# Optimization experiments

Hardware: AMD Instinct MI355X
Metric: run time of the kernel (lower is better)

## Reference

```python
import jax, jax.numpy as jnp
import numpy as np
import math

B, S, D, H = 2, 2048, 1024, 16
DK = D // H


def setup_inputs() -> dict:
    key = jax.random.key(0)
    ks = jax.random.split(key, 8)
    s = 1.0 / math.sqrt(D)
    inp = {
        "query": jax.random.normal(ks[0], (B, S, D), jnp.float32),
        "key": jax.random.normal(ks[1], (B, S, D), jnp.float32),
        "value": jax.random.normal(ks[2], (B, S, D), jnp.float32),
        # causal mask: (1, 1, S, S), 1 where attention allowed
        "mask": jnp.tril(jnp.ones((S, S), jnp.int32))[None, None, :, :],
        "Wq": jax.random.normal(ks[3], (D, D), jnp.float32) * s,
        "Wk": jax.random.normal(ks[4], (D, D), jnp.float32) * s,
        "Wv": jax.random.normal(ks[5], (D, D), jnp.float32) * s,
        "Wo": jax.random.normal(ks[6], (D, D), jnp.float32) * s,
    }
    return inp


def reference(query, key, value, mask, Wq, Wk, Wv, Wo):
    # nn.Linear(bias=False): y = x @ W.T
    def proj_heads(x, W):
        y = jnp.einsum("bsd,ed->bse", x, W)          # (B,S,D)
        return y.reshape(B, -1, H, DK).transpose(0, 2, 1, 3)  # (B,H,S,DK)

    q = proj_heads(query, Wq)
    k = proj_heads(key, Wk)
    v = proj_heads(value, Wv)

    scale = jnp.asarray(math.sqrt(DK), q.dtype)
    scores = jnp.einsum("bhqd,bhkd->bhqk", q, k) / scale  # (B,H,S,S)
    scores = jnp.where(mask == 0, -jnp.inf, scores)
    attn = jax.nn.softmax(scores, axis=-1)
    # dropout p=0.0 (eval): identity
    out = jnp.einsum("bhqk,bhkd->bhqd", attn, v)          # (B,H,S,DK)
    concat = out.transpose(0, 2, 1, 3).reshape(B, -1, D)  # (B,S,D)
    return jnp.einsum("bsd,ed->bse", concat, Wo)
```

## Files before the change

kernel.cpp:

```cpp
#include <hip/hip_runtime.h>
#include <hip/hip_bf16.h>

#define B_ 2
#define S_ 2048
#define D_ 1024
#define H_ 16
#define DK_ 64

typedef __hip_bfloat16 bf16;
typedef __attribute__((ext_vector_type(8))) short bf16x8;
typedef __attribute__((ext_vector_type(4))) short bf16x4;
typedef __attribute__((ext_vector_type(4))) float f32x4;

#define GLDS16(g, l)                                                     \
    __builtin_amdgcn_global_load_lds(                                    \
        (const __attribute__((address_space(1))) void*)(g),              \
        (__attribute__((address_space(3))) void*)(l), 16, 0, 0)

#define MFMA_K32(a, b, c) __builtin_amdgcn_mfma_f32_16x16x32_bf16(a, b, c, 0, 0, 0)
#define MFMA_K16(a, b, c) __builtin_amdgcn_mfma_f32_16x16x16bf16_1k(a, b, c, 0, 0, 0)
#define EXP2F(x) __builtin_amdgcn_exp2f(x)

__global__ __launch_bounds__(256) void cvt_all(
    const float* __restrict__ q, const float* __restrict__ k, const float* __restrict__ v,
    const float* __restrict__ w0, const float* __restrict__ w1,
    const float* __restrict__ w2, const float* __restrict__ w3,
    bf16* __restrict__ oq, bf16* __restrict__ ok, bf16* __restrict__ ov,
    bf16* __restrict__ o0, bf16* __restrict__ o1, bf16* __restrict__ o2,
    bf16* __restrict__ o3) {
    int bid = blockIdx.x;
    const float* src; bf16* dst; int base;
    if      (bid < 2048) { src = q;  dst = oq; base = bid; }
    else if (bid < 4096) { src = k;  dst = ok; base = bid - 2048; }
    else if (bid < 6144) { src = v;  dst = ov; base = bid - 4096; }
    else if (bid < 6656) { src = w0; dst = o0; base = bid - 6144; }
    else if (bid < 7168) { src = w1; dst = o1; base = bid - 6656; }
    else if (bid < 7680) { src = w2; dst = o2; base = bid - 7168; }
    else                 { src = w3; dst = o3; base = bid - 7680; }
    int i = (base * 256 + threadIdx.x) * 8;
    float4 a = *(const float4*)(src + i);
    float4 b = *(const float4*)(src + i + 4);
    __align__(16) bf16 o[8];
    o[0] = __float2bfloat16(a.x); o[1] = __float2bfloat16(a.y);
    o[2] = __float2bfloat16(a.z); o[3] = __float2bfloat16(a.w);
    o[4] = __float2bfloat16(b.x); o[5] = __float2bfloat16(b.y);
    o[6] = __float2bfloat16(b.z); o[7] = __float2bfloat16(b.w);
    *(bf16x8*)(dst + i) = *(const bf16x8*)o;
}

__device__ __forceinline__ void proj_loop32(const bf16* __restrict__ X,
                                            const bf16* __restrict__ W,
                                            int m0, int n0, bf16* As, bf16* Bs,
                                            f32x4 (&acc)[4][4]) {
    const int K = D_;
    const int tid = threadIdx.x;
    const int lane = tid & 63, wave = tid >> 6;
    const int lm = lane & 15, quad = lane >> 4;
    const int wr = wave >> 1, wc = wave & 1;

    auto stage = [&](int t, int bf) {
        int k0 = t * 32;
        bf16* Ab = As + bf * (128 * 32);
        bf16* Bb = Bs + bf * (128 * 32);
#pragma unroll
        for (int i = 0; i < 2; ++i) {
            int s = i * 256 + tid;
            int row = s >> 2, c = (s & 3) ^ (row & 3);
            GLDS16(X + (size_t)(m0 + row) * K + k0 + c * 8, Ab + s * 8);
        }
#pragma unroll
        for (int i = 0; i < 2; ++i) {
            int s = i * 256 + tid;
            int row = s >> 2, c = (s & 3) ^ (row & 3);
            GLDS16(W + (size_t)(n0 + row) * K + k0 + c * 8, Bb + s * 8);
        }
    };

    stage(0, 0);
    for (int t = 0; t < K / 32; ++t) {
        __syncthreads();
        if (t + 1 < K / 32) stage(t + 1, (t + 1) & 1);
        const bf16* Ab = As + (t & 1) * (128 * 32);
        const bf16* Bb = Bs + (t & 1) * (128 * 32);
        bf16x8 aF[4], bF[4];
#pragma unroll
        for (int mt = 0; mt < 4; ++mt) {
            int row = wr * 64 + mt * 16 + lm;
            aF[mt] = *(const bf16x8*)(Ab + row * 32 + ((quad ^ (row & 3)) * 8));
        }
#pragma unroll
        for (int nt = 0; nt < 4; ++nt) {
            int row = wc * 64 + nt * 16 + lm;
            bF[nt] = *(const bf16x8*)(Bb + row * 32 + ((quad ^ (row & 3)) * 8));
        }
#pragma unroll
        for (int mt = 0; mt < 4; ++mt)
#pragma unroll
            for (int nt = 0; nt < 4; ++nt)
                acc[mt][nt] = MFMA_K32(aF[mt], bF[nt], acc[mt][nt]);
    }
}

__global__ __launch_bounds__(256) void proj_qkv(
    const bf16* __restrict__ qx, const bf16* __restrict__ kx, const bf16* __restrict__ vx,
    const bf16* __restrict__ wq, const bf16* __restrict__ wk, const bf16* __restrict__ wv,
    bf16* __restrict__ qb, bf16* __restrict__ kb, bf16* __restrict__ vtb) {
    __shared__ __align__(16) bf16 As[2 * 128 * 32];
    __shared__ __align__(16) bf16 Bs[2 * 128 * 32];
    const int L = (int)blockIdx.x;
    const int tile = (L & 7) * 96 + (L >> 3);
    const int z = tile >> 8;
    const int rem = tile & 255;
    const int n0 = (rem & 7) * 128;
    const int m0 = (rem >> 3) * 128;
    const bf16* X = (z == 0) ? qx : (z == 1) ? kx : vx;
    const bf16* W = (z == 0) ? wq : (z == 1) ? wk : wv;
    f32x4 acc[4][4] = {};
    proj_loop32(X, W, m0, n0, As, Bs, acc);

    const int lane = threadIdx.x & 63, wave = threadIdx.x >> 6;
    const int lm = lane & 15, quad = lane >> 4;
    const int wr = wave >> 1, wc = wave & 1;
#pragma unroll
    for (int mt = 0; mt < 4; ++mt) {
        int mbase = m0 + wr * 64 + mt * 16 + quad * 4;
#pragma unroll
        for (int nt = 0; nt < 4; ++nt) {
            int n = n0 + wc * 64 + nt * 16 + lm;
            if (z == 2) {
                int b = mbase >> 11, s = mbase & (S_ - 1);
                unsigned short u[4];
#pragma unroll
                for (int r = 0; r < 4; ++r) {
                    bf16 hv = __float2bfloat16(acc[mt][nt][r]);
                    u[r] = *(unsigned short*)&hv;
                }
                ushort4 pk = {u[0], u[1], u[2], u[3]};
                *(ushort4*)(vtb + ((size_t)(b * 1024 + n) * S_ + s)) = pk;
            } else {
                bf16* Y = z ? kb : qb;
#pragma unroll
                for (int r = 0; r < 4; ++r)
                    Y[(size_t)(mbase + r) * D_ + n] = __float2bfloat16(acc[mt][nt][r]);
            }
        }
    }
}

__global__ __launch_bounds__(256) void proj_o(const bf16* __restrict__ X,
                                              const bf16* __restrict__ W,
                                              float* __restrict__ Y) {
    __shared__ __align__(16) bf16 As[2 * 128 * 32];
    __shared__ __align__(16) bf16 Bs[2 * 128 * 32];
    const int L = (int)blockIdx.x;
    const int tile = (L & 7) * 32 + (L >> 3);
    const int n0 = (tile & 7) * 128;
    const int m0 = (tile >> 3) * 128;
    f32x4 acc[4][4] = {};
    proj_loop32(X, W, m0, n0, As, Bs, acc);

    const int lane = threadIdx.x & 63, wave = threadIdx.x >> 6;
    const int lm = lane & 15, quad = lane >> 4;
    const int wr = wave >> 1, wc = wave & 1;
#pragma unroll
    for (int mt = 0; mt < 4; ++mt) {
        int mbase = m0 + wr * 64 + mt * 16 + quad * 4;
#pragma unroll
        for (int nt = 0; nt < 4; ++nt) {
            int n = n0 + wc * 64 + nt * 16 + lm;
#pragma unroll
            for (int r = 0; r < 4; ++r)
                Y[(size_t)(mbase + r) * D_ + n] = acc[mt][nt][r];
        }
    }
}

__global__ __launch_bounds__(512) void attn_kernel(const bf16* __restrict__ Q,
                                                   const bf16* __restrict__ Kb,
                                                   const bf16* __restrict__ VT,
                                                   bf16* __restrict__ O) {
    __shared__ __align__(16) bf16 kt[2][128 * 64];
    __shared__ __align__(16) bf16 vt[2][64 * 128];

    const int tid = threadIdx.x;
    const int lane = tid & 63, wave = tid >> 6;
    const int lm = lane & 15, quad = lane >> 4;
    const int f = (int)blockIdx.x;
    const int cls = f & 7;
    const int t = f >> 3;
    const int qi = 15 - (t >> 2);
    const int combo = cls + 8 * (t & 3);
    const int b = combo >> 4, h = combo & 15;
    const int q0 = qi * 128 + wave * 16;

    const size_t bhoff = (size_t)b * S_ * D_ + (size_t)h * DK_;
    const bf16* vtb = VT + ((size_t)b * 1024 + h * DK_) * S_;

    const bf16* qp = Q + bhoff + (size_t)(q0 + lm) * D_ + quad * 8;
    bf16x8 aq0 = *(const bf16x8*)(qp);
    bf16x8 aq1 = *(const bf16x8*)(qp + 32);

    f32x4 oacc[4] = {};
    float lsum = 0.f;
    const float cexp = 0.125f * 1.44269504f;

    auto stage = [&](int i, int bf) {
        int j0s = i * 128;
#pragma unroll
        for (int ii = 0; ii < 2; ++ii) {
            int s = ii * 512 + tid;
            int j = s >> 3, c = (s & 7) ^ (j & 7);
            GLDS16(Kb + bhoff + (size_t)(j0s + j) * D_ + c * 8, kt[bf] + s * 8);
        }
#pragma unroll
        for (int ii = 0; ii < 2; ++ii) {
            int s = ii * 512 + tid;
            int d = s >> 4, c = (s & 15) ^ (d & 15);
            GLDS16(vtb + (size_t)d * S_ + j0s + c * 8, vt[bf] + s * 8);
        }
    };

    auto chunk = [&](const bf16* ktb, const bf16* vtl, int st, bool mk) {
        int j = st * 16 + lm;
        bf16x8 bk0 = *(const bf16x8*)(ktb + (((j << 3) | (quad ^ (j & 7))) * 8));
        bf16x8 bk1 = *(const bf16x8*)(ktb + (((j << 3) | ((4 + quad) ^ (j & 7))) * 8));
        f32x4 z = {};
        z = MFMA_K32(bk0, aq0, z);
        z = MFMA_K32(bk1, aq1, z);
        bf16x4 pa;
        float rs = 0.f;
#pragma unroll
        for (int r = 0; r < 4; ++r) {
            float p = EXP2F(z[r] * cexp);
            if (mk && (quad * 4 + r > lm)) p = 0.f;
            rs += p;
            bf16 hv = __float2bfloat16(p);
            pa[r] = *(short*)&hv;
        }
        lsum += rs;
#pragma unroll
        for (int dt = 0; dt < 4; ++dt) {
            int d = dt * 16 + lm;
            int cl = st * 2 + (quad >> 1);
            bf16x4 bv = *(const bf16x4*)(vtl + d * 128 +
                                         ((cl ^ (d & 15)) * 8 + (quad & 1) * 4));
            oacc[dt] = MFMA_K16(pa, bv, oacc[dt]);
        }
    };

    stage(0, 0);

    for (int i = 0; i <= qi; ++i) {
        __syncthreads();
        if (i < qi) stage(i + 1, (i + 1) & 1);
        const bf16* ktb = kt[i & 1];
        const bf16* vtl = vt[i & 1];
        if (i < qi) {
#pragma unroll
            for (int st = 0; st < 8; ++st) chunk(ktb, vtl, st, false);
        } else {
            for (int st = 0; st < wave; ++st) chunk(ktb, vtl, st, false);
            chunk(ktb, vtl, wave, true);
        }
    }

    float l = lsum;
    l += __shfl_xor(l, 16, 64);
    l += __shfl_xor(l, 32, 64);
#pragma unroll
    for (int r = 0; r < 4; ++r) {
        float inv = 1.f / __shfl(l, quad * 4 + r, 64);
        int qrow = q0 + quad * 4 + r;
#pragma unroll
        for (int dt = 0; dt < 4; ++dt) {
            int d = dt * 16 + lm;
            O[bhoff + (size_t)qrow * D_ + d] = __float2bfloat16(oacc[dt][r] * inv);
        }
    }
}

extern "C" void kernel_launch(void* const* d_in, const int* in_sizes, int n_in,
                              void* d_out, int out_size, void* d_ws, size_t ws_size,
                              hipStream_t stream) {
    const float* q_in = (const float*)d_in[0];
    const float* k_in = (const float*)d_in[1];
    const float* v_in = (const float*)d_in[2];
    const float* Wq_f = (const float*)d_in[4];
    const float* Wk_f = (const float*)d_in[5];
    const float* Wv_f = (const float*)d_in[6];
    const float* Wo_f = (const float*)d_in[7];
    float* out = (float*)d_out;

    const size_t NEL = (size_t)B_ * S_ * D_;
    const size_t WEL = (size_t)D_ * D_;
    bf16* p = (bf16*)d_ws;
    bf16* qx = p;  p += NEL;
    bf16* kx = p;  p += NEL;
    bf16* vx = p;  p += NEL;
    bf16* wq = p;  p += WEL;
    bf16* wk = p;  p += WEL;
    bf16* wv = p;  p += WEL;
    bf16* wo = p;  p += WEL;
    bf16* qb = p;  p += NEL;
    bf16* kb = p;  p += NEL;
    bf16* vtb = p; p += NEL;
    bf16* cb = p;  p += NEL;

    cvt_all<<<8192, 256, 0, stream>>>(q_in, k_in, v_in, Wq_f, Wk_f, Wv_f, Wo_f,
                                      qx, kx, vx, wq, wk, wv, wo);

    proj_qkv<<<dim3(768), 256, 0, stream>>>(qx, kx, vx, wq, wk, wv, qb, kb, vtb);

    attn_kernel<<<dim3(512), 512, 0, stream>>>(qb, kb, vtb, cb);

    proj_o<<<dim3(256), 256, 0, stream>>>(cb, wo, out);
}
```

Measured before the change: 225.6 us.

## Retile output projection to 64-row tiles, rebalance attention order, add MFMA priority

The output projection now uses 64x128 tiles with its own double-buffered LDS loop. This doubles the block count to 512 so more compute units are busy. The attention kernel reorders which query tiles the second half of blocks process, so short and long causal tiles interleave more evenly. It also raises wave priority around the MFMA sections. Smaller tiles lower data reuse per block, and setprio may not change scheduling.

```diff
diff --git a/kernel.cpp b/kernel.cpp
--- a/kernel.cpp
+++ b/kernel.cpp
@@ -150,21 +150,65 @@
 __global__ __launch_bounds__(256) void proj_o(const bf16* __restrict__ X,
                                               const bf16* __restrict__ W,
                                               float* __restrict__ Y) {
-    __shared__ __align__(16) bf16 As[2 * 128 * 32];
+    __shared__ __align__(16) bf16 As[2 * 64 * 32];
     __shared__ __align__(16) bf16 Bs[2 * 128 * 32];
     const int L = (int)blockIdx.x;
-    const int tile = (L & 7) * 32 + (L >> 3);
+    const int tile = (L & 7) * 64 + (L >> 3);
     const int n0 = (tile & 7) * 128;
-    const int m0 = (tile >> 3) * 128;
-    f32x4 acc[4][4] = {};
-    proj_loop32(X, W, m0, n0, As, Bs, acc);
-
-    const int lane = threadIdx.x & 63, wave = threadIdx.x >> 6;
+    const int m0 = (tile >> 3) * 64;
+
+    const int K = D_;
+    const int tid = threadIdx.x;
+    const int lane = tid & 63, wave = tid >> 6;
     const int lm = lane & 15, quad = lane >> 4;
     const int wr = wave >> 1, wc = wave & 1;
-#pragma unroll
-    for (int mt = 0; mt < 4; ++mt) {
-        int mbase = m0 + wr * 64 + mt * 16 + quad * 4;
+
+    f32x4 acc[2][4] = {};
+
+    auto stage = [&](int t, int bf) {
+        int k0 = t * 32;
+        bf16* Ab = As + bf * (64 * 32);
+        bf16* Bb = Bs + bf * (128 * 32);
+        {
+            int s = tid;
+            int row = s >> 2, c = (s & 3) ^ (row & 3);
+            GLDS16(X + (size_t)(m0 + row) * K + k0 + c * 8, Ab + s * 8);
+        }
+#pragma unroll
+        for (int i = 0; i < 2; ++i) {
+            int s = i * 256 + tid;
+            int row = s >> 2, c = (s & 3) ^ (row & 3);
+            GLDS16(W + (size_t)(n0 + row) * K + k0 + c * 8, Bb + s * 8);
+        }
+    };
+
+    stage(0, 0);
+    for (int t = 0; t < K / 32; ++t) {
+        __syncthreads();
+        if (t + 1 < K / 32) stage(t + 1, (t + 1) & 1);
+        const bf16* Ab = As + (t & 1) * (64 * 32);
+        const bf16* Bb = Bs + (t & 1) * (128 * 32);
+        bf16x8 aF[2], bF[4];
+#pragma unroll
+        for (int mt = 0; mt < 2; ++mt) {
+            int row = wr * 32 + mt * 16 + lm;
+            aF[mt] = *(const bf16x8*)(Ab + row * 32 + ((quad ^ (row & 3)) * 8));
+        }
+#pragma unroll
+        for (int nt = 0; nt < 4; ++nt) {
+            int row = wc * 64 + nt * 16 + lm;
+            bF[nt] = *(const bf16x8*)(Bb + row * 32 + ((quad ^ (row & 3)) * 8));
+        }
+#pragma unroll
+        for (int mt = 0; mt < 2; ++mt)
+#pragma unroll
+            for (int nt = 0; nt < 4; ++nt)
+                acc[mt][nt] = MFMA_K32(aF[mt], bF[nt], acc[mt][nt]);
+    }
+
+#pragma unroll
+    for (int mt = 0; mt < 2; ++mt) {
+        int mbase = m0 + wr * 32 + mt * 16 + quad * 4;
 #pragma unroll
         for (int nt = 0; nt < 4; ++nt) {
             int n = n0 + wc * 64 + nt * 16 + lm;
@@ -188,7 +232,7 @@
     const int f = (int)blockIdx.x;
     const int cls = f & 7;
     const int t = f >> 3;
-    const int qi = 15 - (t >> 2);
+    const int qi = (t < 32) ? (15 - (t >> 2)) : ((t >> 2) - 8);
     const int combo = cls + 8 * (t & 3);
     const int b = combo >> 4, h = combo & 15;
     const int q0 = qi * 128 + wave * 16;
@@ -225,8 +269,10 @@
         bf16x8 bk0 = *(const bf16x8*)(ktb + (((j << 3) | (quad ^ (j & 7))) * 8));
         bf16x8 bk1 = *(const bf16x8*)(ktb + (((j << 3) | ((4 + quad) ^ (j & 7))) * 8));
         f32x4 z = {};
+        __builtin_amdgcn_s_setprio(1);
         z = MFMA_K32(bk0, aq0, z);
         z = MFMA_K32(bk1, aq1, z);
+        __builtin_amdgcn_s_setprio(0);
         bf16x4 pa;
         float rs = 0.f;
 #pragma unroll
@@ -238,6 +284,7 @@
             pa[r] = *(short*)&hv;
         }
         lsum += rs;
+        __builtin_amdgcn_s_setprio(1);
 #pragma unroll
         for (int dt = 0; dt < 4; ++dt) {
             int d = dt * 16 + lm;
@@ -246,6 +293,7 @@
                                          ((cl ^ (d & 15)) * 8 + (quad & 1) * 4));
             oacc[dt] = MFMA_K16(pa, bv, oacc[dt]);
         }
+        __builtin_amdgcn_s_setprio(0);
     };
 
     stage(0, 0);
@@ -313,5 +361,5 @@
 
     attn_kernel<<<dim3(512), 512, 0, stream>>>(qb, kb, vtb, cb);
 
-    proj_o<<<dim3(256), 256, 0, stream>>>(cb, wo, out);
-}
+    proj_o<<<dim3(512), 256, 0, stream>>>(cb, wo, out);
+}
```

Result: no change. 221.6 us (-1.8%).
